# Performance work log

Hardware: AMD Instinct MI355X
Metric: run time of the kernel (lower is better)

The kernel has to match this reference:

```python
import jax, jax.numpy as jnp
import numpy as np

D = 1024
H = 16
DH = D // H

def setup_inputs() -> dict:
    key = jax.random.key(0)
    ks = jax.random.split(key, 9)
    s = 0.02
    return {
        "x": jax.random.normal(ks[0], (2, 2048, D), dtype=jnp.float32),
        "Wq": jax.random.normal(ks[1], (D, D), dtype=jnp.float32) * s,
        "bq": jnp.zeros((D,), dtype=jnp.float32),
        "Wk": jax.random.normal(ks[2], (D, D), dtype=jnp.float32) * s,
        "bk": jnp.zeros((D,), dtype=jnp.float32),
        "Wv": jax.random.normal(ks[3], (D, D), dtype=jnp.float32) * s,
        "bv": jnp.zeros((D,), dtype=jnp.float32),
        "Wo": jax.random.normal(ks[4], (D, D), dtype=jnp.float32) * s,
        "bo": jnp.zeros((D,), dtype=jnp.float32),
    }

def reference(x, Wq, bq, Wk, bk, Wv, bv, Wo, bo):
    B, S, Dm = x.shape
    def proj(W, b):
        # [B,S,D] -> [B,H,S,DH]
        return (x @ W + b).reshape(B, S, H, DH).transpose(0, 2, 1, 3)
    q = proj(Wq, bq)
    k = proj(Wk, bk)
    v = proj(Wv, bv)
    scale = 1.0 / np.sqrt(DH).astype(np.float32)
    raw = jnp.einsum('bhsd,bhtd->bhst', q, k) * scale  # [B,H,S,S]
    w = jax.nn.softmax(raw, axis=-1)
    out = jnp.einsum('bhst,bhtd->bhsd', w, v)          # [B,H,S,DH]
    out = out.transpose(0, 2, 1, 3).reshape(B, S, Dm)
    return out @ Wo + bo
```

## Files before the change

kernel.cpp:

```cpp
#include <hip/hip_runtime.h>
#include <math.h>

constexpr int Dm  = 1024;
constexpr int NH  = 16;
constexpr int SQ  = 2048;
constexpr int NB  = 2;

typedef float f32x4 __attribute__((ext_vector_type(4)));
typedef float f32x16 __attribute__((ext_vector_type(16)));
typedef short bf16x8 __attribute__((ext_vector_type(8)));
typedef __attribute__((address_space(3))) unsigned int lds_u32;
typedef __attribute__((address_space(1))) const unsigned int glb_u32;

__device__ __forceinline__ void gload_lds16(const void* g, void* l) {
    __builtin_amdgcn_global_load_lds((glb_u32*)(uintptr_t)g, (lds_u32*)(uintptr_t)l, 16, 0, 0);
}

__device__ __forceinline__ unsigned short bf_round(float x) {
    unsigned u = __float_as_uint(x);
    unsigned r = u + 0x7fffu + ((u >> 16) & 1u);
    return (unsigned short)(r >> 16);
}

__device__ __forceinline__ float exp2_fast(float x) {
    float r;
    asm("v_exp_f32 %0, %1" : "=v"(r) : "v"(x));
    return r;
}

__device__ __forceinline__ unsigned cvt_pk(float lo, float hi_) {
    unsigned r;
    asm("v_cvt_pk_bf16_f32 %0, %1, %2" : "=v"(r) : "v"(lo), "v"(hi_));
    return r;
}

__device__ __forceinline__ void permlane_swap(unsigned& a, unsigned& b) {
    asm volatile("v_permlane32_swap_b32 %0, %1" : "+v"(a), "+v"(b));
}

__device__ __forceinline__ bf16x8 make_frag(unsigned a, unsigned b, unsigned c, unsigned d) {
    union { unsigned u[4]; bf16x8 v; } uu;
    uu.u[0] = a; uu.u[1] = b; uu.u[2] = c; uu.u[3] = d;
    return uu.v;
}

__global__ __launch_bounds__(256) void cvt_bf16(const float* __restrict__ in,
                                                unsigned short* __restrict__ out) {
    size_t i = ((size_t)blockIdx.x * 256 + threadIdx.x) * 8;
    float4 a = *(const float4*)&in[i];
    float4 b = *(const float4*)&in[i + 4];
    unsigned short o8[8] __attribute__((aligned(16)));
    o8[0] = bf_round(a.x); o8[1] = bf_round(a.y); o8[2] = bf_round(a.z); o8[3] = bf_round(a.w);
    o8[4] = bf_round(b.x); o8[5] = bf_round(b.y); o8[6] = bf_round(b.z); o8[7] = bf_round(b.w);
    *(uint4*)&out[i] = *(const uint4*)o8;
}

__global__ __launch_bounds__(256) void trans_w(const float* __restrict__ Wq,
                                               const float* __restrict__ Wk,
                                               const float* __restrict__ Wv,
                                               const float* __restrict__ Wo,
                                               unsigned short* __restrict__ wt) {
    const int z = blockIdx.z;
    const float* W = (z == 0) ? Wq : (z == 1) ? Wk : (z == 2) ? Wv : Wo;
    unsigned short* dst = wt + (size_t)z * Dm * Dm;
    __shared__ float T[64][65];
    const int k0 = blockIdx.x * 64, n0 = blockIdx.y * 64;
    const int tid = threadIdx.x;
#pragma unroll
    for (int i = 0; i < 4; ++i) {
        int s = tid + i * 256;
        int kk = s >> 4, c = (s & 15) * 4;
        *(float4*)&T[kk][c] = *(const float4*)&W[(size_t)(k0 + kk) * Dm + n0 + c];
    }
    __syncthreads();
#pragma unroll
    for (int i = 0; i < 2; ++i) {
        int s = tid + i * 256;
        int n = s >> 3, c8 = (s & 7) * 8;
        unsigned short o8[8] __attribute__((aligned(16)));
#pragma unroll
        for (int j = 0; j < 8; ++j) o8[j] = bf_round(T[c8 + j][n]);
        *(uint4*)&dst[(size_t)(n0 + n) * Dm + k0 + c8] = *(const uint4*)o8;
    }
}

__global__ __launch_bounds__(512) void gemm_qkv8(
    const unsigned short* __restrict__ xb,
    const unsigned short* __restrict__ wt,
    const float* __restrict__ bq, const float* __restrict__ bk,
    const float* __restrict__ bv,
    unsigned short* __restrict__ qbuf, unsigned short* __restrict__ kbuf,
    unsigned short* __restrict__ vtbuf)
{
    __shared__ unsigned short Alds[2][256 * 64];
    __shared__ unsigned short Blds[2][256 * 64];

    const int tid = threadIdx.x;
    const int lane = tid & 63, wid = tid >> 6;
    const int wm = wid >> 2, wn = wid & 3;
    const int l15 = lane & 15, lg = lane >> 4;

    const int bid = blockIdx.x;
    const int swz = (bid & 7) * 24 + (bid >> 3);
    const int bx = swz % 12, by = swz / 12;
    const int m0 = by * 256, n0 = bx * 256;

    const int srow = wid * 8 + (lane >> 3);
    const int scol = ((lane & 7) ^ ((lane >> 3) & 7)) * 8;

    const unsigned short* Abase = xb + (size_t)m0 * Dm;
    const unsigned short* Bbase = wt + (size_t)n0 * Dm;

#define STAGE_TILE(t)                                                              \
    do {                                                                           \
        const unsigned short* As_ = Abase + (t) * 64;                              \
        const unsigned short* Bs_ = Bbase + (t) * 64;                              \
        unsigned short* Ad_ = Alds[(t) & 1];                                       \
        unsigned short* Bd_ = Blds[(t) & 1];                                       \
        _Pragma("unroll")                                                          \
        for (int i_ = 0; i_ < 4; ++i_) {                                           \
            gload_lds16(&As_[(size_t)(i_ * 64 + srow) * Dm + scol],                \
                        &Ad_[i_ * 4096 + wid * 512]);                              \
            gload_lds16(&Bs_[(size_t)(i_ * 64 + srow) * Dm + scol],                \
                        &Bd_[i_ * 4096 + wid * 512]);                              \
        }                                                                          \
    } while (0)

    f32x4 acc[8][4];
#pragma unroll
    for (int mr = 0; mr < 8; ++mr)
#pragma unroll
        for (int nr = 0; nr < 4; ++nr) acc[mr][nr] = (f32x4){0.f, 0.f, 0.f, 0.f};

    STAGE_TILE(0);
    asm volatile("s_waitcnt vmcnt(0)" ::: "memory");
    __builtin_amdgcn_s_barrier();

    for (int t = 0; t < Dm / 64; ++t) {
        unsigned short* Ad = Alds[t & 1];
        unsigned short* Bd = Blds[t & 1];
        if (t + 1 < Dm / 64) STAGE_TILE(t + 1);

        bf16x8 a_[4][2], b_[2][2];

#define RD_A(qm, fr, ks) \
    (*(const bf16x8*)&Ad[(wm * 128 + (qm) * 64 + (fr) * 16 + l15) * 64 + \
                         ((((ks) * 4 + lg) ^ (l15 & 7)) * 8)])
#define RD_B(qn, fc, ks) \
    (*(const bf16x8*)&Bd[(wn * 64 + (qn) * 32 + (fc) * 16 + l15) * 64 + \
                         ((((ks) * 4 + lg) ^ (l15 & 7)) * 8)])

#pragma unroll
        for (int fr = 0; fr < 4; ++fr) {
            a_[fr][0] = RD_A(0, fr, 0); a_[fr][1] = RD_A(0, fr, 1);
        }
#pragma unroll
        for (int fc = 0; fc < 2; ++fc) {
            b_[fc][0] = RD_B(0, fc, 0); b_[fc][1] = RD_B(0, fc, 1);
        }
        __builtin_amdgcn_s_barrier();
        __builtin_amdgcn_s_setprio(1);
#pragma unroll
        for (int fr = 0; fr < 4; ++fr)
#pragma unroll
            for (int fc = 0; fc < 2; ++fc)
#pragma unroll
                for (int ks = 0; ks < 2; ++ks)
                    acc[fr][fc] = __builtin_amdgcn_mfma_f32_16x16x32_bf16(
                        a_[fr][ks], b_[fc][ks], acc[fr][fc], 0, 0, 0);
        __builtin_amdgcn_s_setprio(0);
        __builtin_amdgcn_s_barrier();

#pragma unroll
        for (int fc = 0; fc < 2; ++fc) {
            b_[fc][0] = RD_B(1, fc, 0); b_[fc][1] = RD_B(1, fc, 1);
        }
        __builtin_amdgcn_s_barrier();
        __builtin_amdgcn_s_setprio(1);
#pragma unroll
        for (int fr = 0; fr < 4; ++fr)
#pragma unroll
            for (int fc = 0; fc < 2; ++fc)
#pragma unroll
                for (int ks = 0; ks < 2; ++ks)
                    acc[fr][2 + fc] = __builtin_amdgcn_mfma_f32_16x16x32_bf16(
                        a_[fr][ks], b_[fc][ks], acc[fr][2 + fc], 0, 0, 0);
        __builtin_amdgcn_s_setprio(0);
        __builtin_amdgcn_s_barrier();

#pragma unroll
        for (int fr = 0; fr < 4; ++fr) {
            a_[fr][0] = RD_A(1, fr, 0); a_[fr][1] = RD_A(1, fr, 1);
        }
        __builtin_amdgcn_s_barrier();
        __builtin_amdgcn_s_setprio(1);
#pragma unroll
        for (int fr = 0; fr < 4; ++fr)
#pragma unroll
            for (int fc = 0; fc < 2; ++fc)
#pragma unroll
                for (int ks = 0; ks < 2; ++ks)
                    acc[4 + fr][2 + fc] = __builtin_amdgcn_mfma_f32_16x16x32_bf16(
                        a_[fr][ks], b_[fc][ks], acc[4 + fr][2 + fc], 0, 0, 0);
        __builtin_amdgcn_s_setprio(0);
        __builtin_amdgcn_s_barrier();

#pragma unroll
        for (int fc = 0; fc < 2; ++fc) {
            b_[fc][0] = RD_B(0, fc, 0); b_[fc][1] = RD_B(0, fc, 1);
        }
        __builtin_amdgcn_s_barrier();
        __builtin_amdgcn_s_setprio(1);
#pragma unroll
        for (int fr = 0; fr < 4; ++fr)
#pragma unroll
            for (int fc = 0; fc < 2; ++fc)
#pragma unroll
                for (int ks = 0; ks < 2; ++ks)
                    acc[4 + fr][fc] = __builtin_amdgcn_mfma_f32_16x16x32_bf16(
                        a_[fr][ks], b_[fc][ks], acc[4 + fr][fc], 0, 0, 0);
        __builtin_amdgcn_s_setprio(0);
        __builtin_amdgcn_s_barrier();

        asm volatile("s_waitcnt vmcnt(0)" ::: "memory");
        __builtin_amdgcn_s_barrier();
#undef RD_A
#undef RD_B
    }

    const int zsel = n0 >> 10;
    const int nz0 = (n0 & 1023) + wn * 64;
    const float* bias = (zsel == 0) ? bq : (zsel == 1) ? bk : bv;
    const float scale = 0.18033688011f;

#pragma unroll
    for (int mr = 0; mr < 8; ++mr) {
#pragma unroll
        for (int nr = 0; nr < 4; ++nr) {
            const int m = m0 + wm * 128 + mr * 16 + lg * 4;
            const int nz = nz0 + nr * 16 + l15;
            const float bb_ = bias[nz];
            if (zsel == 0) {
#pragma unroll
                for (int rr = 0; rr < 4; ++rr)
                    qbuf[(size_t)(m + rr) * Dm + nz] =
                        bf_round((acc[mr][nr][rr] + bb_) * scale);
            } else if (zsel == 1) {
#pragma unroll
                for (int rr = 0; rr < 4; ++rr)
                    kbuf[(size_t)(m + rr) * Dm + nz] = bf_round(acc[mr][nr][rr] + bb_);
            } else {
                const int bbv = m >> 11, s = m & (SQ - 1);
                const int hh = nz >> 6, d = nz & 63;
                unsigned short p4[4] __attribute__((aligned(8)));
#pragma unroll
                for (int rr = 0; rr < 4; ++rr) p4[rr] = bf_round(acc[mr][nr][rr] + bb_);
                *(uint2*)&vtbuf[(((size_t)bbv * NH + hh) * 64 + d) * SQ + s] =
                    *(const uint2*)p4;
            }
        }
    }
#undef STAGE_TILE
}

__device__ __forceinline__ void gemm_main(const unsigned short* __restrict__ A,
                                          const unsigned short* __restrict__ Bt,
                                          unsigned short* As, unsigned short* Bs,
                                          int m0, int n0, f32x4 acc[4][4]) {
    const int tid = threadIdx.x;
    const int lane = tid & 63, wid = tid >> 6;
    const int l15 = lane & 15, lg = lane >> 4;
    const int wr = (wid >> 1) * 64, wc = (wid & 1) * 64;

    for (int k0 = 0; k0 < Dm; k0 += 64) {
#pragma unroll
        for (int i = 0; i < 4; ++i) {
            int row = i * 32 + (tid >> 3);
            int sc8 = (tid & 7) * 8;
            int lbase = i * 2048 + wid * 512;
            gload_lds16(&A[(size_t)(m0 + row) * Dm + k0 + sc8], &As[lbase]);
            gload_lds16(&Bt[(size_t)(n0 + row) * Dm + k0 + sc8], &Bs[lbase]);
        }
        __syncthreads();
#pragma unroll
        for (int ks = 0; ks < 2; ++ks) {
            bf16x8 af[4], bfr[4];
#pragma unroll
            for (int r = 0; r < 4; ++r)
                af[r] = *(const bf16x8*)&As[(wr + r * 16 + l15) * 64 + ks * 32 + lg * 8];
#pragma unroll
            for (int c = 0; c < 4; ++c)
                bfr[c] = *(const bf16x8*)&Bs[(wc + c * 16 + l15) * 64 + ks * 32 + lg * 8];
#pragma unroll
            for (int r = 0; r < 4; ++r)
#pragma unroll
                for (int c = 0; c < 4; ++c)
                    acc[r][c] = __builtin_amdgcn_mfma_f32_16x16x32_bf16(af[r], bfr[c],
                                                                        acc[r][c], 0, 0, 0);
        }
        __syncthreads();
    }
}

__global__ __launch_bounds__(256) void gemm_out(const unsigned short* __restrict__ A,
                                                const unsigned short* __restrict__ Bt,
                                                const float* __restrict__ bias,
                                                float* __restrict__ Cf) {
    __shared__ unsigned short As[128 * 64];
    __shared__ unsigned short Bs[128 * 64];
    const int m0 = blockIdx.y * 128, n0 = blockIdx.x * 128;

    f32x4 acc[4][4];
#pragma unroll
    for (int r = 0; r < 4; ++r)
#pragma unroll
        for (int c = 0; c < 4; ++c) acc[r][c] = (f32x4){0.f, 0.f, 0.f, 0.f};

    gemm_main(A, Bt, As, Bs, m0, n0, acc);

    const int tid = threadIdx.x, lane = tid & 63, wid = tid >> 6;
    const int l15 = lane & 15, lg = lane >> 4;
    const int wr = (wid >> 1) * 64, wc = (wid & 1) * 64;
#pragma unroll
    for (int r = 0; r < 4; ++r) {
#pragma unroll
        for (int c = 0; c < 4; ++c) {
            const int mBase = m0 + wr + r * 16 + lg * 4;
            const int n = n0 + wc + c * 16 + l15;
            const float bv_ = bias[n];
#pragma unroll
            for (int rr = 0; rr < 4; ++rr)
                Cf[(size_t)(mBase + rr) * Dm + n] = acc[r][c][rr] + bv_;
        }
    }
}

__global__ __launch_bounds__(256) void attn_bf16(const unsigned short* q,
                                                 const unsigned short* __restrict__ k,
                                                 const unsigned short* __restrict__ vt,
                                                 unsigned short* ao) {
    __shared__ unsigned short KVs[2][2][64 * 64];
    const int qt = blockIdx.x, h = blockIdx.y, b = blockIdx.z;
    const int tid = threadIdx.x, lane = tid & 63, wid = tid >> 6;
    const int l31 = lane & 31, hi = lane >> 5;

    const size_t qrow0 = (size_t)b * SQ + qt * 128;
    const unsigned short* qp = q + (qrow0 + wid * 32 + l31) * Dm + h * 64;
    bf16x8 qf[4];
#pragma unroll
    for (int ks = 0; ks < 4; ++ks)
        qf[ks] = *(const bf16x8*)&qp[ks * 16 + hi * 8];

    const unsigned short* kb = k + (size_t)b * SQ * Dm + h * 64;
    const unsigned short* vb = vt + ((size_t)b * NH + h) * 64 * SQ;

    const int row0 = tid >> 3;
    const int s8 = (tid & 7) * 8;
    const int sw8 = (((tid & 7) ^ (row0 & 7))) * 8;
    const int koff0 = row0 * 64 + sw8;
    const int koff1 = (row0 + 32) * 64 + sw8;

    {
        uint4 k0v = *(const uint4*)&kb[(size_t)row0 * Dm + s8];
        uint4 k1v = *(const uint4*)&kb[(size_t)(row0 + 32) * Dm + s8];
        uint4 v0v = *(const uint4*)&vb[(size_t)row0 * SQ + s8];
        uint4 v1v = *(const uint4*)&vb[(size_t)(row0 + 32) * SQ + s8];
        *(uint4*)&KVs[0][0][koff0] = k0v; *(uint4*)&KVs[0][0][koff1] = k1v;
        *(uint4*)&KVs[0][1][koff0] = v0v; *(uint4*)&KVs[0][1][koff1] = v1v;
    }
    __syncthreads();

    float psum = 0.f;
    f32x16 c0, c1;
#pragma unroll
    for (int i = 0; i < 16; ++i) { c0[i] = 0.f; c1[i] = 0.f; }

    int cur = 0;
    for (int t0 = 0; t0 < SQ; t0 += 64) {
        const bool hasNext = (t0 + 64) < SQ;
        uint4 kr0, kr1, vr0, vr1;
        if (hasNext) {
            const unsigned short* kn = kb + (size_t)(t0 + 64) * Dm;
            const unsigned short* vn = vb + (t0 + 64);
            kr0 = *(const uint4*)&kn[(size_t)row0 * Dm + s8];
            kr1 = *(const uint4*)&kn[(size_t)(row0 + 32) * Dm + s8];
            vr0 = *(const uint4*)&vn[(size_t)row0 * SQ + s8];
            vr1 = *(const uint4*)&vn[(size_t)(row0 + 32) * SQ + s8];
        }
        const unsigned short* Kc = KVs[cur][0];
        const unsigned short* Vc = KVs[cur][1];

#pragma unroll
        for (int kblk = 0; kblk < 2; ++kblk) {
            f32x16 p;
#pragma unroll
            for (int i = 0; i < 16; ++i) p[i] = 0.f;
            __builtin_amdgcn_s_setprio(1);
#pragma unroll
            for (int ks = 0; ks < 4; ++ks) {
                int row = kblk * 32 + l31;
                int slot = ((ks * 2 + hi) ^ (l31 & 7)) * 8;
                bf16x8 kf = *(const bf16x8*)&Kc[row * 64 + slot];
                p = __builtin_amdgcn_mfma_f32_32x32x16_bf16(kf, qf[ks], p, 0, 0, 0);
            }
            __builtin_amdgcn_s_setprio(0);

            float e[16];
#pragma unroll
            for (int i = 0; i < 16; ++i) { e[i] = exp2_fast(p[i]); psum += e[i]; }
            unsigned w0 = cvt_pk(e[0], e[1]),   w1 = cvt_pk(e[2], e[3]);
            unsigned w2 = cvt_pk(e[4], e[5]),   w3 = cvt_pk(e[6], e[7]);
            unsigned w4 = cvt_pk(e[8], e[9]),   w5 = cvt_pk(e[10], e[11]);
            unsigned w6 = cvt_pk(e[12], e[13]), w7 = cvt_pk(e[14], e[15]);
            permlane_swap(w0, w2); permlane_swap(w1, w3);
            permlane_swap(w4, w6); permlane_swap(w5, w7);
            bf16x8 pf0 = make_frag(w0, w1, w2, w3);
            bf16x8 pf1 = make_frag(w4, w5, w6, w7);

            int s0 = ((kblk * 4 + hi) ^ (l31 & 7)) * 8;
            int s1 = ((kblk * 4 + 2 + hi) ^ (l31 & 7)) * 8;
            bf16x8 va0 = *(const bf16x8*)&Vc[l31 * 64 + s0];
            bf16x8 va1 = *(const bf16x8*)&Vc[l31 * 64 + s1];
            bf16x8 vb0 = *(const bf16x8*)&Vc[(32 + l31) * 64 + s0];
            bf16x8 vb1 = *(const bf16x8*)&Vc[(32 + l31) * 64 + s1];
            __builtin_amdgcn_s_setprio(1);
            c0 = __builtin_amdgcn_mfma_f32_32x32x16_bf16(va0, pf0, c0, 0, 0, 0);
            c0 = __builtin_amdgcn_mfma_f32_32x32x16_bf16(va1, pf1, c0, 0, 0, 0);
            c1 = __builtin_amdgcn_mfma_f32_32x32x16_bf16(vb0, pf0, c1, 0, 0, 0);
            c1 = __builtin_amdgcn_mfma_f32_32x32x16_bf16(vb1, pf1, c1, 0, 0, 0);
            __builtin_amdgcn_s_setprio(0);
        }

        if (hasNext) {
            unsigned short* Kn = KVs[cur ^ 1][0];
            unsigned short* Vn = KVs[cur ^ 1][1];
            *(uint4*)&Kn[koff0] = kr0; *(uint4*)&Kn[koff1] = kr1;
            *(uint4*)&Vn[koff0] = vr0; *(uint4*)&Vn[koff1] = vr1;
        }
        __syncthreads();
        cur ^= 1;
    }

    float s = psum + __shfl_xor(psum, 32, 64);
    float inv = 1.f / s;

    unsigned short* Olds = (unsigned short*)KVs;
    {
        const int orow = wid * 32 + l31;
#pragma unroll
        for (int db = 0; db < 2; ++db) {
#pragma unroll
            for (int i = 0; i < 8; ++i) {
                float lo  = (db ? c1[2 * i] : c0[2 * i]) * inv;
                float hi_ = (db ? c1[2 * i + 1] : c0[2 * i + 1]) * inv;
                unsigned w = cvt_pk(lo, hi_);
                int d7 = hi * 4 + (i & 1) * 2;
                int slot = db * 4 + (i >> 1);
                int sw = slot ^ (l31 & 7);
                *(unsigned*)&Olds[orow * 64 + sw * 8 + d7] = w;
            }
        }
    }
    __syncthreads();
    {
        int r = tid >> 1, half = tid & 1;
        unsigned short* dst = ao + (qrow0 + r) * Dm + h * 64 + half * 32;
#pragma unroll
        for (int j = 0; j < 4; ++j) {
            int slot = half * 4 + j;
            int sw = slot ^ (r & 7);
            *(uint4*)&dst[j * 8] = *(const uint4*)&Olds[r * 64 + sw * 8];
        }
    }
}

extern "C" void kernel_launch(void* const* d_in, const int* in_sizes, int n_in,
                              void* d_out, int out_size, void* d_ws, size_t ws_size,
                              hipStream_t stream) {
    const float* x  = (const float*)d_in[0];
    const float* Wq = (const float*)d_in[1];
    const float* bq = (const float*)d_in[2];
    const float* Wk = (const float*)d_in[3];
    const float* bk = (const float*)d_in[4];
    const float* Wv = (const float*)d_in[5];
    const float* bv = (const float*)d_in[6];
    const float* Wo = (const float*)d_in[7];
    const float* bo = (const float*)d_in[8];
    float* out = (float*)d_out;

    const size_t M = (size_t)NB * SQ;
    const size_t elems = M * Dm;
    unsigned short* xb    = (unsigned short*)d_ws;
    unsigned short* wtb   = xb + elems;
    unsigned short* qbuf  = wtb + 4ull * Dm * Dm;
    unsigned short* kbuf  = qbuf + elems;
    unsigned short* vtbuf = kbuf + elems;

    dim3 blk(256);
    hipLaunchKernelGGL(cvt_bf16, dim3(elems / (256 * 8)), blk, 0, stream, x, xb);
    hipLaunchKernelGGL(trans_w, dim3(16, 16, 4), blk, 0, stream, Wq, Wk, Wv, Wo, wtb);

    hipLaunchKernelGGL(gemm_qkv8, dim3(192), dim3(512), 0, stream,
                       xb, wtb, bq, bk, bv, qbuf, kbuf, vtbuf);

    hipLaunchKernelGGL(attn_bf16, dim3(SQ / 128, NH, NB), blk, 0, stream,
                       qbuf, kbuf, vtbuf, qbuf);

    hipLaunchKernelGGL(gemm_out, dim3(Dm / 128, M / 128), blk, 0, stream,
                       qbuf, wtb + 3ull * Dm * Dm, bo, out);
}
```

Before: 128.3 us.

## Merge prologue kernels, retile QKV GEMM to 256x192, compute softmax sums via MFMA

Fuses the x-to-bf16 conversion and the weight transpose into one prologue launch, removing a kernel launch. The QKV projection GEMM changes from 192 blocks of 256x256 tiles to 256 blocks of 256x192 tiles, so the grid matches the CU count better, and the bias/scale selection moves to per-column. In attention, the row sum of probabilities is computed by an extra MFMA against a ones fragment instead of scalar adds plus a cross-lane shuffle. This trades extra MFMA work for fewer VALU ops, and the sum is now taken over bf16-rounded values.

```diff
diff --git a/kernel.cpp b/kernel.cpp
--- a/kernel.cpp
+++ b/kernel.cpp
@@ -44,28 +44,33 @@
     return uu.v;
 }
 
-__global__ __launch_bounds__(256) void cvt_bf16(const float* __restrict__ in,
-                                                unsigned short* __restrict__ out) {
-    size_t i = ((size_t)blockIdx.x * 256 + threadIdx.x) * 8;
-    float4 a = *(const float4*)&in[i];
-    float4 b = *(const float4*)&in[i + 4];
-    unsigned short o8[8] __attribute__((aligned(16)));
-    o8[0] = bf_round(a.x); o8[1] = bf_round(a.y); o8[2] = bf_round(a.z); o8[3] = bf_round(a.w);
-    o8[4] = bf_round(b.x); o8[5] = bf_round(b.y); o8[6] = bf_round(b.z); o8[7] = bf_round(b.w);
-    *(uint4*)&out[i] = *(const uint4*)o8;
-}
-
-__global__ __launch_bounds__(256) void trans_w(const float* __restrict__ Wq,
-                                               const float* __restrict__ Wk,
-                                               const float* __restrict__ Wv,
-                                               const float* __restrict__ Wo,
-                                               unsigned short* __restrict__ wt) {
+__global__ __launch_bounds__(256) void prologue(const float* __restrict__ x,
+                                                const float* __restrict__ Wq,
+                                                const float* __restrict__ Wk,
+                                                const float* __restrict__ Wv,
+                                                const float* __restrict__ Wo,
+                                                unsigned short* __restrict__ xb,
+                                                unsigned short* __restrict__ wt) {
     const int z = blockIdx.z;
+    const int tid = threadIdx.x;
+    if (z == 4) {
+        size_t base = ((size_t)blockIdx.y * 16 + blockIdx.x) * 16384;
+#pragma unroll
+        for (int it = 0; it < 8; ++it) {
+            size_t i = base + (size_t)it * 2048 + (size_t)tid * 8;
+            float4 a = *(const float4*)&x[i];
+            float4 b = *(const float4*)&x[i + 4];
+            unsigned short o8[8] __attribute__((aligned(16)));
+            o8[0] = bf_round(a.x); o8[1] = bf_round(a.y); o8[2] = bf_round(a.z); o8[3] = bf_round(a.w);
+            o8[4] = bf_round(b.x); o8[5] = bf_round(b.y); o8[6] = bf_round(b.z); o8[7] = bf_round(b.w);
+            *(uint4*)&xb[i] = *(const uint4*)o8;
+        }
+        return;
+    }
     const float* W = (z == 0) ? Wq : (z == 1) ? Wk : (z == 2) ? Wv : Wo;
     unsigned short* dst = wt + (size_t)z * Dm * Dm;
     __shared__ float T[64][65];
     const int k0 = blockIdx.x * 64, n0 = blockIdx.y * 64;
-    const int tid = threadIdx.x;
 #pragma unroll
     for (int i = 0; i < 4; ++i) {
         int s = tid + i * 256;
@@ -84,7 +89,7 @@
     }
 }
 
-__global__ __launch_bounds__(512) void gemm_qkv8(
+__global__ __launch_bounds__(512) void gemm_qkv192(
     const unsigned short* __restrict__ xb,
     const unsigned short* __restrict__ wt,
     const float* __restrict__ bq, const float* __restrict__ bk,
@@ -93,7 +98,7 @@
     unsigned short* __restrict__ vtbuf)
 {
     __shared__ unsigned short Alds[2][256 * 64];
-    __shared__ unsigned short Blds[2][256 * 64];
+    __shared__ unsigned short Blds[2][192 * 64];
 
     const int tid = threadIdx.x;
     const int lane = tid & 63, wid = tid >> 6;
@@ -101,9 +106,9 @@
     const int l15 = lane & 15, lg = lane >> 4;
 
     const int bid = blockIdx.x;
-    const int swz = (bid & 7) * 24 + (bid >> 3);
-    const int bx = swz % 12, by = swz / 12;
-    const int m0 = by * 256, n0 = bx * 256;
+    const int swz = (bid & 7) * 32 + (bid >> 3);
+    const int bx = swz & 15, by = swz >> 4;
+    const int m0 = by * 256, n0 = bx * 192;
 
     const int srow = wid * 8 + (lane >> 3);
     const int scol = ((lane & 7) ^ ((lane >> 3) & 7)) * 8;
@@ -118,19 +123,20 @@
         unsigned short* Ad_ = Alds[(t) & 1];                                       \
         unsigned short* Bd_ = Blds[(t) & 1];                                       \
         _Pragma("unroll")                                                          \
-        for (int i_ = 0; i_ < 4; ++i_) {                                           \
+        for (int i_ = 0; i_ < 4; ++i_)                                             \
             gload_lds16(&As_[(size_t)(i_ * 64 + srow) * Dm + scol],                \
                         &Ad_[i_ * 4096 + wid * 512]);                              \
+        _Pragma("unroll")                                                          \
+        for (int i_ = 0; i_ < 3; ++i_)                                             \
             gload_lds16(&Bs_[(size_t)(i_ * 64 + srow) * Dm + scol],                \
                         &Bd_[i_ * 4096 + wid * 512]);                              \
-        }                                                                          \
     } while (0)
 
-    f32x4 acc[8][4];
+    f32x4 acc[8][3];
 #pragma unroll
     for (int mr = 0; mr < 8; ++mr)
 #pragma unroll
-        for (int nr = 0; nr < 4; ++nr) acc[mr][nr] = (f32x4){0.f, 0.f, 0.f, 0.f};
+        for (int nr = 0; nr < 3; ++nr) acc[mr][nr] = (f32x4){0.f, 0.f, 0.f, 0.f};
 
     STAGE_TILE(0);
     asm volatile("s_waitcnt vmcnt(0)" ::: "memory");
@@ -141,13 +147,13 @@
         unsigned short* Bd = Blds[t & 1];
         if (t + 1 < Dm / 64) STAGE_TILE(t + 1);
 
-        bf16x8 a_[4][2], b_[2][2];
+        bf16x8 a_[4][2], b01[2][2], b2[2];
 
 #define RD_A(qm, fr, ks) \
     (*(const bf16x8*)&Ad[(wm * 128 + (qm) * 64 + (fr) * 16 + l15) * 64 + \
                          ((((ks) * 4 + lg) ^ (l15 & 7)) * 8)])
-#define RD_B(qn, fc, ks) \
-    (*(const bf16x8*)&Bd[(wn * 64 + (qn) * 32 + (fc) * 16 + l15) * 64 + \
+#define RD_B(fc, ks) \
+    (*(const bf16x8*)&Bd[(wn * 48 + (fc) * 16 + l15) * 64 + \
                          ((((ks) * 4 + lg) ^ (l15 & 7)) * 8)])
 
 #pragma unroll
@@ -156,7 +162,7 @@
         }
 #pragma unroll
         for (int fc = 0; fc < 2; ++fc) {
-            b_[fc][0] = RD_B(0, fc, 0); b_[fc][1] = RD_B(0, fc, 1);
+            b01[fc][0] = RD_B(fc, 0); b01[fc][1] = RD_B(fc, 1);
         }
         __builtin_amdgcn_s_barrier();
         __builtin_amdgcn_s_setprio(1);
@@ -167,24 +173,19 @@
 #pragma unroll
                 for (int ks = 0; ks < 2; ++ks)
                     acc[fr][fc] = __builtin_amdgcn_mfma_f32_16x16x32_bf16(
-                        a_[fr][ks], b_[fc][ks], acc[fr][fc], 0, 0, 0);
+                        a_[fr][ks], b01[fc][ks], acc[fr][fc], 0, 0, 0);
         __builtin_amdgcn_s_setprio(0);
         __builtin_amdgcn_s_barrier();
 
-#pragma unroll
-        for (int fc = 0; fc < 2; ++fc) {
-            b_[fc][0] = RD_B(1, fc, 0); b_[fc][1] = RD_B(1, fc, 1);
-        }
+        b2[0] = RD_B(2, 0); b2[1] = RD_B(2, 1);
         __builtin_amdgcn_s_barrier();
         __builtin_amdgcn_s_setprio(1);
 #pragma unroll
         for (int fr = 0; fr < 4; ++fr)
 #pragma unroll
-            for (int fc = 0; fc < 2; ++fc)
-#pragma unroll
-                for (int ks = 0; ks < 2; ++ks)
-                    acc[fr][2 + fc] = __builtin_amdgcn_mfma_f32_16x16x32_bf16(
-                        a_[fr][ks], b_[fc][ks], acc[fr][2 + fc], 0, 0, 0);
+            for (int ks = 0; ks < 2; ++ks)
+                acc[fr][2] = __builtin_amdgcn_mfma_f32_16x16x32_bf16(
+                    a_[fr][ks], b2[ks], acc[fr][2], 0, 0, 0);
         __builtin_amdgcn_s_setprio(0);
         __builtin_amdgcn_s_barrier();
 
@@ -197,17 +198,15 @@
 #pragma unroll
         for (int fr = 0; fr < 4; ++fr)
 #pragma unroll
-            for (int fc = 0; fc < 2; ++fc)
-#pragma unroll
-                for (int ks = 0; ks < 2; ++ks)
-                    acc[4 + fr][2 + fc] = __builtin_amdgcn_mfma_f32_16x16x32_bf16(
-                        a_[fr][ks], b_[fc][ks], acc[4 + fr][2 + fc], 0, 0, 0);
+            for (int ks = 0; ks < 2; ++ks)
+                acc[4 + fr][2] = __builtin_amdgcn_mfma_f32_16x16x32_bf16(
+                    a_[fr][ks], b2[ks], acc[4 + fr][2], 0, 0, 0);
         __builtin_amdgcn_s_setprio(0);
         __builtin_amdgcn_s_barrier();
 
 #pragma unroll
         for (int fc = 0; fc < 2; ++fc) {
-            b_[fc][0] = RD_B(0, fc, 0); b_[fc][1] = RD_B(0, fc, 1);
+            b01[fc][0] = RD_B(fc, 0); b01[fc][1] = RD_B(fc, 1);
         }
         __builtin_amdgcn_s_barrier();
         __builtin_amdgcn_s_setprio(1);
@@ -218,7 +217,7 @@
 #pragma unroll
                 for (int ks = 0; ks < 2; ++ks)
                     acc[4 + fr][fc] = __builtin_amdgcn_mfma_f32_16x16x32_bf16(
-                        a_[fr][ks], b_[fc][ks], acc[4 + fr][fc], 0, 0, 0);
+                        a_[fr][ks], b01[fc][ks], acc[4 + fr][fc], 0, 0, 0);
         __builtin_amdgcn_s_setprio(0);
         __builtin_amdgcn_s_barrier();
 
@@ -228,24 +227,23 @@
 #undef RD_B
     }
 
-    const int zsel = n0 >> 10;
-    const int nz0 = (n0 & 1023) + wn * 64;
-    const float* bias = (zsel == 0) ? bq : (zsel == 1) ? bk : bv;
-    const float scale = 0.18033688011f;
-
+    const float qscale = 0.18033688011f;
 #pragma unroll
     for (int mr = 0; mr < 8; ++mr) {
 #pragma unroll
-        for (int nr = 0; nr < 4; ++nr) {
+        for (int nr = 0; nr < 3; ++nr) {
             const int m = m0 + wm * 128 + mr * 16 + lg * 4;
-            const int nz = nz0 + nr * 16 + l15;
+            const int nglob = n0 + wn * 48 + nr * 16 + l15;
+            const int zq = nglob >> 10;
+            const int nz = nglob & 1023;
+            const float* bias = (zq == 0) ? bq : (zq == 1) ? bk : bv;
             const float bb_ = bias[nz];
-            if (zsel == 0) {
+            if (zq == 0) {
 #pragma unroll
                 for (int rr = 0; rr < 4; ++rr)
                     qbuf[(size_t)(m + rr) * Dm + nz] =
-                        bf_round((acc[mr][nr][rr] + bb_) * scale);
-            } else if (zsel == 1) {
+                        bf_round((acc[mr][nr][rr] + bb_) * qscale);
+            } else if (zq == 1) {
 #pragma unroll
                 for (int rr = 0; rr < 4; ++rr)
                     kbuf[(size_t)(m + rr) * Dm + nz] = bf_round(acc[mr][nr][rr] + bb_);
@@ -370,10 +368,10 @@
     }
     __syncthreads();
 
-    float psum = 0.f;
-    f32x16 c0, c1;
-#pragma unroll
-    for (int i = 0; i < 16; ++i) { c0[i] = 0.f; c1[i] = 0.f; }
+    const bf16x8 ones = make_frag(0x3F803F80u, 0x3F803F80u, 0x3F803F80u, 0x3F803F80u);
+    f32x16 c0, c1, c2;
+#pragma unroll
+    for (int i = 0; i < 16; ++i) { c0[i] = 0.f; c1[i] = 0.f; c2[i] = 0.f; }
 
     int cur = 0;
     for (int t0 = 0; t0 < SQ; t0 += 64) {
@@ -407,7 +405,7 @@
 
             float e[16];
 #pragma unroll
-            for (int i = 0; i < 16; ++i) { e[i] = exp2_fast(p[i]); psum += e[i]; }
+            for (int i = 0; i < 16; ++i) e[i] = exp2_fast(p[i]);
             unsigned w0 = cvt_pk(e[0], e[1]),   w1 = cvt_pk(e[2], e[3]);
             unsigned w2 = cvt_pk(e[4], e[5]),   w3 = cvt_pk(e[6], e[7]);
             unsigned w4 = cvt_pk(e[8], e[9]),   w5 = cvt_pk(e[10], e[11]);
@@ -425,9 +423,11 @@
             bf16x8 vb1 = *(const bf16x8*)&Vc[(32 + l31) * 64 + s1];
             __builtin_amdgcn_s_setprio(1);
             c0 = __builtin_amdgcn_mfma_f32_32x32x16_bf16(va0, pf0, c0, 0, 0, 0);
+            c1 = __builtin_amdgcn_mfma_f32_32x32x16_bf16(vb0, pf0, c1, 0, 0, 0);
+            c2 = __builtin_amdgcn_mfma_f32_32x32x16_bf16(ones, pf0, c2, 0, 0, 0);
             c0 = __builtin_amdgcn_mfma_f32_32x32x16_bf16(va1, pf1, c0, 0, 0, 0);
-            c1 = __builtin_amdgcn_mfma_f32_32x32x16_bf16(vb0, pf0, c1, 0, 0, 0);
             c1 = __builtin_amdgcn_mfma_f32_32x32x16_bf16(vb1, pf1, c1, 0, 0, 0);
+            c2 = __builtin_amdgcn_mfma_f32_32x32x16_bf16(ones, pf1, c2, 0, 0, 0);
             __builtin_amdgcn_s_setprio(0);
         }
 
@@ -441,8 +441,7 @@
         cur ^= 1;
     }
 
-    float s = psum + __shfl_xor(psum, 32, 64);
-    float inv = 1.f / s;
+    float inv = 1.f / c2[0];
 
     unsigned short* Olds = (unsigned short*)KVs;
     {
@@ -497,10 +496,10 @@
     unsigned short* vtbuf = kbuf + elems;
 
     dim3 blk(256);
-    hipLaunchKernelGGL(cvt_bf16, dim3(elems / (256 * 8)), blk, 0, stream, x, xb);
-    hipLaunchKernelGGL(trans_w, dim3(16, 16, 4), blk, 0, stream, Wq, Wk, Wv, Wo, wtb);
-
-    hipLaunchKernelGGL(gemm_qkv8, dim3(192), dim3(512), 0, stream,
+    hipLaunchKernelGGL(prologue, dim3(16, 16, 5), blk, 0, stream,
+                       x, Wq, Wk, Wv, Wo, xb, wtb);
+
+    hipLaunchKernelGGL(gemm_qkv192, dim3(256), dim3(512), 0, stream,
                        xb, wtb, bq, bk, bv, qbuf, kbuf, vtbuf);
 
     hipLaunchKernelGGL(attn_bf16, dim3(SQ / 128, NH, NB), blk, 0, stream,
```

After: 123.3 us. 3.9% less time.
